# Kernel tuning notes

Hardware: AMD Instinct MI355X
Metric: run time of the kernel (lower is better)

Reference implementation:

```python
import jax, jax.numpy as jnp
import numpy as np

LN_EPS = 1e-5
N_FREQ = 10
D_TIME = 64
FIELD_DIMS = [(63, 128), (128, 128), (128, 3)]  # (d_in, d_out) per generated layer


def gelu(x):
    return jax.nn.gelu(x, approximate=False)  # torch default exact GELU


def ln(x, g, b):
    m = x.mean(-1, keepdims=True)
    v = ((x - m) ** 2).mean(-1, keepdims=True)
    return (x - m) / jnp.sqrt(v + LN_EPS) * g + b


def lin(x, w, b):
    return x @ w.T + b


def setup_inputs():
    key = jax.random.key(0)
    it = iter(jax.random.split(key, 64))

    def W(o, i, s=0.02):
        return jax.random.normal(next(it), (o, i), dtype=jnp.float32) * s

    inp = {}
    inp["points"] = jax.random.normal(next(it), (32, 16384, 3), dtype=jnp.float32)
    inp["t"] = jax.random.uniform(next(it), (32,), dtype=jnp.float32)
    # PointNet encoder: mlp1 = Lin(3,128)+LN+GELU+Lin(128,128)+LN+GELU
    inp["pn_w1"], inp["pn_b1"] = W(128, 3), jnp.zeros(128)
    inp["pn_g1"], inp["pn_be1"] = jnp.ones(128), jnp.zeros(128)
    inp["pn_w2"], inp["pn_b2"] = W(128, 128), jnp.zeros(128)
    inp["pn_g2"], inp["pn_be2"] = jnp.ones(128), jnp.zeros(128)
    # mlp2 = Lin(128,256)+LN+GELU+Lin(256,256)+LN
    inp["pn_w3"], inp["pn_b3"] = W(256, 128), jnp.zeros(256)
    inp["pn_g3"], inp["pn_be3"] = jnp.ones(256), jnp.zeros(256)
    inp["pn_w4"], inp["pn_b4"] = W(256, 256), jnp.zeros(256)
    inp["pn_g4"], inp["pn_be4"] = jnp.ones(256), jnp.zeros(256)
    # HyperNetwork context_proj: Lin(256+64,256)+LN+GELU+Lin(256,256)+LN+GELU
    inp["hp_w1"], inp["hp_b1"] = W(256, 320), jnp.zeros(256)
    inp["hp_g1"], inp["hp_be1"] = jnp.ones(256), jnp.zeros(256)
    inp["hp_w2"], inp["hp_b2"] = W(256, 256), jnp.zeros(256)
    inp["hp_g2"], inp["hp_be2"] = jnp.ones(256), jnp.zeros(256)
    # weight/bias generators for field dims [63,128,128,3]
    for i, (din, dout) in enumerate(FIELD_DIMS):
        inp[f"wg{i}_w"] = W(din * dout, 256)
        inp[f"wg{i}_b"] = jnp.zeros(din * dout)
        inp[f"bg{i}_w"] = W(dout, 256)
        inp[f"bg{i}_b"] = jnp.zeros(dout)
    return inp


def reference(points, t,
              pn_w1, pn_b1, pn_g1, pn_be1, pn_w2, pn_b2, pn_g2, pn_be2,
              pn_w3, pn_b3, pn_g3, pn_be3, pn_w4, pn_b4, pn_g4, pn_be4,
              hp_w1, hp_b1, hp_g1, hp_be1, hp_w2, hp_b2, hp_g2, hp_be2,
              wg0_w, wg0_b, bg0_w, bg0_b,
              wg1_w, wg1_b, bg1_w, bg1_b,
              wg2_w, wg2_b, bg2_w, bg2_b):
    B = points.shape[0]
    # ---- PointNet encoder -> global context [B, 256]
    h = gelu(ln(lin(points, pn_w1, pn_b1), pn_g1, pn_be1))
    h = gelu(ln(lin(h, pn_w2, pn_b2), pn_g2, pn_be2))
    h = gelu(ln(lin(h, pn_w3, pn_b3), pn_g3, pn_be3))
    h = ln(lin(h, pn_w4, pn_b4), pn_g4, pn_be4)
    ctx = h.max(axis=1)
    # ---- sinusoidal time embedding [B, 64]
    half = D_TIME // 2
    emb = jnp.exp(jnp.arange(half, dtype=jnp.float32) * (-np.log(10000.0) / (half - 1)))
    te = t[:, None] * emb
    te = jnp.concatenate([jnp.sin(te), jnp.cos(te)], axis=-1)
    # ---- hypernetwork context projection [B, 256]
    c = jnp.concatenate([ctx, te], axis=-1)
    c = gelu(ln(lin(c, hp_w1, hp_b1), hp_g1, hp_be1))
    c = gelu(ln(lin(c, hp_w2, hp_b2), hp_g2, hp_be2))
    # ---- Fourier position encoding [B, N, 63]
    freqs = (2.0 ** jnp.arange(N_FREQ, dtype=jnp.float32)) * jnp.pi
    xf = (points[..., None] * freqs).reshape(points.shape[0], points.shape[1], -1)
    pe = jnp.concatenate([points, jnp.sin(xf), jnp.cos(xf)], axis=-1)
    # ---- generate per-sample weights, apply field MLP
    gens = [(wg0_w, wg0_b, bg0_w, bg0_b), (wg1_w, wg1_b, bg1_w, bg1_b), (wg2_w, wg2_b, bg2_w, bg2_b)]
    x = pe
    n_layers = len(FIELD_DIMS)
    for i, ((din, dout), (wgw, wgb, bgw, bgb)) in enumerate(zip(FIELD_DIMS, gens)):
        w = lin(c, wgw, wgb).reshape(B, dout, din)
        w = w / jnp.maximum(jnp.linalg.norm(w, axis=-1, keepdims=True), 1e-12)  # F.normalize
        b = lin(c, bgw, bgb)
        x = jnp.einsum('bnd,bod->bno', x, w) + b[:, None, :]
        if i < n_layers - 1:
            x = gelu(x)
    return x  # [B, N, 3] velocities
```

## Files before the change

### kernel.cpp

```cpp
#include <hip/hip_runtime.h>

typedef _Float16 f16;
typedef f16 f16x8 __attribute__((ext_vector_type(8)));
typedef f16 f16x4 __attribute__((ext_vector_type(4)));
typedef float f32x4 __attribute__((ext_vector_type(4)));

#define N_PTS 16384
#define NBATCH 32
#define PTILE 64
#define PN_BLOCKS (N_PTS / PTILE)

__device__ __forceinline__ float gelu_exact(float x) {
    return 0.5f * x * (1.0f + erff(x * 0.70710678118654752440f));
}
__device__ __forceinline__ float gelu_fast(float x) {
    float u = x * x;
    float t = x * fmaf(u, 0.07135481627f, 1.5957691216f);
    float e = __expf(-t);
    return __fdividef(x, 1.f + e);
}
__device__ __forceinline__ unsigned fkey(float x) {
    unsigned u = __float_as_uint(x);
    return (u & 0x80000000u) ? ~u : (u | 0x80000000u);
}
__device__ __forceinline__ float funkey(unsigned k) {
    return (k & 0x80000000u) ? __uint_as_float(k ^ 0x80000000u) : __uint_as_float(~k);
}

template<int ACOLS, int DIN, int DOUT, int MODE>
__device__ __forceinline__ void mfma_layerT(
    f16 (*A)[ACOLS],
    const f16* __restrict__ Wg, const float* __restrict__ Bias,
    const float* __restrict__ Gam, const float* __restrict__ Bet,
    float2 (*Pp)[4], unsigned* __restrict__ mk)
{
    constexpr int KS = DIN / 32, TN = DOUT / 64;
    const int tid = threadIdx.x;
    const int w = tid >> 6, lane = tid & 63;
    const int i15 = lane & 15, g = lane >> 4;

    f32x4 d[4][TN];
#pragma unroll
    for (int nt = 0; nt < 4; ++nt)
#pragma unroll
        for (int mt = 0; mt < TN; ++mt) d[nt][mt] = (f32x4){0.f, 0.f, 0.f, 0.f};

#pragma unroll 2
    for (int ks = 0; ks < KS; ++ks) {
        f16x8 wf[TN];
#pragma unroll
        for (int mt = 0; mt < TN; ++mt)
            wf[mt] = *(const f16x8*)&Wg[(size_t)((w * TN + mt) * 16 + i15) * DIN + ks * 32 + g * 8];
#pragma unroll
        for (int nt = 0; nt < 4; ++nt) {
            f16x8 af = *(const f16x8*)&A[nt * 16 + i15][ks * 32 + g * 8];
#pragma unroll
            for (int mt = 0; mt < TN; ++mt)
                d[nt][mt] = __builtin_amdgcn_mfma_f32_16x16x32_f16(wf[mt], af, d[nt][mt], 0, 0, 0);
        }
    }

    float bi[TN][4], ga[TN][4], be[TN][4];
#pragma unroll
    for (int mt = 0; mt < TN; ++mt) {
        int cb = (w * TN + mt) * 16 + g * 4;
        *(float4*)bi[mt] = *(const float4*)&Bias[cb];
        if constexpr (MODE <= 1) {
            *(float4*)ga[mt] = *(const float4*)&Gam[cb];
            *(float4*)be[mt] = *(const float4*)&Bet[cb];
        }
    }
#pragma unroll
    for (int nt = 0; nt < 4; ++nt)
#pragma unroll
        for (int mt = 0; mt < TN; ++mt)
#pragma unroll
            for (int r = 0; r < 4; ++r) d[nt][mt][r] += bi[mt][r];

    if constexpr (MODE <= 1) {
#pragma unroll
        for (int nt = 0; nt < 4; ++nt) {
            float ss = 0.f, qq = 0.f;
#pragma unroll
            for (int mt = 0; mt < TN; ++mt)
#pragma unroll
                for (int r = 0; r < 4; ++r) {
                    float v = d[nt][mt][r];
                    ss += v; qq += v * v;
                }
            ss += __shfl_xor(ss, 16); qq += __shfl_xor(qq, 16);
            ss += __shfl_xor(ss, 32); qq += __shfl_xor(qq, 32);
            if (g == 0) Pp[nt * 16 + i15][w] = make_float2(ss, qq);
        }
        __syncthreads();
        float mx[TN][4];
        if constexpr (MODE == 1) {
#pragma unroll
            for (int mt = 0; mt < TN; ++mt)
#pragma unroll
                for (int r = 0; r < 4; ++r) mx[mt][r] = -1e30f;
        }
#pragma unroll
        for (int nt = 0; nt < 4; ++nt) {
            int pt = nt * 16 + i15;
            float4 pa = *(const float4*)&Pp[pt][0];
            float4 pb = *(const float4*)&Pp[pt][2];
            float S = pa.x + pa.z + pb.x + pb.z;
            float Q = pa.y + pa.w + pb.y + pb.w;
            float mean = S * (1.f / DOUT);
            float var = Q * (1.f / DOUT) - mean * mean;
            float rstd = rsqrtf(var + 1e-5f);
#pragma unroll
            for (int mt = 0; mt < TN; ++mt) {
                if constexpr (MODE == 0) {
                    f16x4 pk;
#pragma unroll
                    for (int r = 0; r < 4; ++r) {
                        float y = (d[nt][mt][r] - mean) * rstd * ga[mt][r] + be[mt][r];
                        pk[r] = (f16)gelu_fast(y);
                    }
                    *(f16x4*)&A[pt][(w * TN + mt) * 16 + g * 4] = pk;
                } else {
#pragma unroll
                    for (int r = 0; r < 4; ++r) {
                        float y = (d[nt][mt][r] - mean) * rstd * ga[mt][r] + be[mt][r];
                        mx[mt][r] = fmaxf(mx[mt][r], y);
                    }
                }
            }
        }
        if constexpr (MODE == 0) {
            __syncthreads();
        } else {
#pragma unroll
            for (int mt = 0; mt < TN; ++mt)
#pragma unroll
                for (int r = 0; r < 4; ++r) {
                    float m = mx[mt][r];
                    m = fmaxf(m, __shfl_xor(m, 1));
                    m = fmaxf(m, __shfl_xor(m, 2));
                    m = fmaxf(m, __shfl_xor(m, 4));
                    m = fmaxf(m, __shfl_xor(m, 8));
                    mx[mt][r] = m;
                }
            if (i15 == 0) {
#pragma unroll
                for (int mt = 0; mt < TN; ++mt)
#pragma unroll
                    for (int r = 0; r < 4; ++r)
                        atomicMax(&mk[(w * TN + mt) * 16 + g * 4 + r], fkey(mx[mt][r]));
            }
        }
    } else {
        __syncthreads();
#pragma unroll
        for (int nt = 0; nt < 4; ++nt) {
            int pt = nt * 16 + i15;
#pragma unroll
            for (int mt = 0; mt < TN; ++mt) {
                f16x4 pk;
#pragma unroll
                for (int r = 0; r < 4; ++r)
                    pk[r] = (f16)gelu_fast(d[nt][mt][r]);
                *(f16x4*)&A[pt][(w * TN + mt) * 16 + g * 4] = pk;
            }
        }
        __syncthreads();
    }
}

__global__ void init_kernel(unsigned* __restrict__ maxkey) {
    maxkey[blockIdx.x * 256 + threadIdx.x] = 0u;
}

__global__ void prep_kernel(const float* __restrict__ W1, const float* __restrict__ W2,
                            const float* __restrict__ W3, const float* __restrict__ W4,
                            f16* __restrict__ W1f, f16* __restrict__ W2f,
                            f16* __restrict__ W3f, f16* __restrict__ W4f) {
    int i = blockIdx.x * 256 + threadIdx.x;
    if (i < 128 * 32) {
        int r = i >> 5, c = i & 31;
        W1f[i] = (f16)(c < 3 ? W1[r * 3 + c] : 0.f);
    }
    int j = i - 128 * 32;
    if (j >= 0 && j < 128 * 128) W2f[j] = (f16)W2[j];
    int k = i - (128 * 32 + 128 * 128);
    if (k >= 0 && k < 256 * 128) W3f[k] = (f16)W3[k];
    int l = i - (128 * 32 + 128 * 128 + 256 * 128);
    if (l >= 0 && l < 256 * 256) W4f[l] = (f16)W4[l];
}

__global__ __launch_bounds__(256, 3)
void pointnet_kernel(const float* __restrict__ points,
                     const f16* __restrict__ W1f, const float* __restrict__ B1,
                     const float* __restrict__ G1, const float* __restrict__ E1,
                     const f16* __restrict__ W2f, const float* __restrict__ B2,
                     const float* __restrict__ G2, const float* __restrict__ E2,
                     const f16* __restrict__ W3f, const float* __restrict__ B3,
                     const float* __restrict__ G3, const float* __restrict__ E3,
                     const f16* __restrict__ W4f, const float* __restrict__ B4,
                     const float* __restrict__ G4, const float* __restrict__ E4,
                     unsigned* __restrict__ maxkey) {
    __shared__ __attribute__((aligned(16))) f16 A[PTILE][264];
    __shared__ float2 Pp[PTILE][4];
    const int b = blockIdx.x / PN_BLOCKS;
    const int n0 = (blockIdx.x % PN_BLOCKS) * PTILE;
    const int tid = threadIdx.x;
    for (int i = tid; i < PTILE * 32; i += 256) {
        int p = i >> 5, c = i & 31;
        A[p][c] = (f16)(c < 3 ? points[((size_t)b * N_PTS + n0 + p) * 3 + c] : 0.f);
    }
    __syncthreads();
    mfma_layerT<264, 32, 128, 0>(A, W1f, B1, G1, E1, Pp, nullptr);
    mfma_layerT<264, 128, 128, 0>(A, W2f, B2, G2, E2, Pp, nullptr);
    mfma_layerT<264, 128, 256, 0>(A, W3f, B3, G3, E3, Pp, nullptr);
    mfma_layerT<264, 256, 256, 1>(A, W4f, B4, G4, E4, Pp, maxkey + b * 256);
}

__global__ __launch_bounds__(256)
void hyper_kernel(const unsigned* __restrict__ maxkey, const float* __restrict__ tt,
                  const float* __restrict__ HW1, const float* __restrict__ HB1,
                  const float* __restrict__ HG1, const float* __restrict__ HE1,
                  const float* __restrict__ HW2, const float* __restrict__ HB2,
                  const float* __restrict__ HG2, const float* __restrict__ HE2,
                  float* __restrict__ c_out) {
    __shared__ float xc[320];
    __shared__ float buf[256];
    __shared__ float rs[4], rq[4];
    const int b = blockIdx.x, tid = threadIdx.x;
    xc[tid] = funkey(maxkey[b * 256 + tid]);
    if (tid < 32) {
        float emb = expf((float)tid * (-logf(10000.f) / 31.f));
        float arg = tt[b] * emb;
        xc[256 + tid] = sinf(arg);
        xc[288 + tid] = cosf(arg);
    }
    __syncthreads();
    float acc = HB1[tid];
    for (int i = 0; i < 320; i += 4) {
        float4 w = *(const float4*)&HW1[(size_t)tid * 320 + i];
        acc += xc[i] * w.x + xc[i + 1] * w.y + xc[i + 2] * w.z + xc[i + 3] * w.w;
    }
    float s = acc, q = acc * acc;
#pragma unroll
    for (int off = 32; off; off >>= 1) { s += __shfl_xor(s, off); q += __shfl_xor(q, off); }
    if ((tid & 63) == 0) { rs[tid >> 6] = s; rq[tid >> 6] = q; }
    __syncthreads();
    s = rs[0] + rs[1] + rs[2] + rs[3];
    q = rq[0] + rq[1] + rq[2] + rq[3];
    float mean = s * (1.f / 256), var = q * (1.f / 256) - mean * mean;
    float rstd = rsqrtf(var + 1e-5f);
    float h = gelu_exact((acc - mean) * rstd * HG1[tid] + HE1[tid]);
    __syncthreads();
    buf[tid] = h;
    __syncthreads();
    acc = HB2[tid];
    for (int i = 0; i < 256; i += 4) {
        float4 w = *(const float4*)&HW2[(size_t)tid * 256 + i];
        acc += buf[i] * w.x + buf[i + 1] * w.y + buf[i + 2] * w.z + buf[i + 3] * w.w;
    }
    s = acc; q = acc * acc;
#pragma unroll
    for (int off = 32; off; off >>= 1) { s += __shfl_xor(s, off); q += __shfl_xor(q, off); }
    if ((tid & 63) == 0) { rs[tid >> 6] = s; rq[tid >> 6] = q; }
    __syncthreads();
    s = rs[0] + rs[1] + rs[2] + rs[3];
    q = rq[0] + rq[1] + rq[2] + rq[3];
    mean = s * (1.f / 256); var = q * (1.f / 256) - mean * mean;
    rstd = rsqrtf(var + 1e-5f);
    c_out[b * 256 + tid] = gelu_exact((acc - mean) * rstd * HG2[tid] + HE2[tid]);
}

__device__ __forceinline__ void gen_row(float acc[32], const float (*cs)[256],
                                        const float* __restrict__ Wg,
                                        const float* __restrict__ Wgb, int f, bool valid) {
#pragma unroll
    for (int b = 0; b < 32; ++b) acc[b] = 0.f;
    if (!valid) return;
    for (int i = 0; i < 256; i += 4) {
        float4 w = *(const float4*)&Wg[(size_t)f * 256 + i];
#pragma unroll
        for (int b = 0; b < 32; ++b) {
            float4 cv = *(const float4*)&cs[b][i];
            acc[b] += cv.x * w.x + cv.y * w.y + cv.z * w.z + cv.w * w.w;
        }
    }
    float bias = Wgb[f];
#pragma unroll
    for (int b = 0; b < 32; ++b) acc[b] += bias;
}

__global__ __launch_bounds__(256)
void wgen_kernel(const float* __restrict__ c,
                 const float* __restrict__ WG0, const float* __restrict__ WGB0,
                 const float* __restrict__ BG0, const float* __restrict__ BGB0,
                 const float* __restrict__ WG1, const float* __restrict__ WGB1,
                 const float* __restrict__ BG1, const float* __restrict__ BGB1,
                 const float* __restrict__ WG2, const float* __restrict__ WGB2,
                 const float* __restrict__ BG2, const float* __restrict__ BGB2,
                 f16* __restrict__ w0f, f16* __restrict__ w1f, f16* __restrict__ w2f,
                 float* __restrict__ bb0, float* __restrict__ bb1, float* __restrict__ bb2) {
    __shared__ float cs[32][256];
    const int tid = threadIdx.x;
    for (int i = tid; i < 32 * 256; i += 256) cs[i >> 8][i & 255] = c[i];
    __syncthreads();
    const int wave = tid >> 6, lane = tid & 63;
    const int task = blockIdx.x * 4 + wave;
    if (task >= 262) return;

    float accA[32], accB[32];
    if (task < 259) {
        int layer, o;
        if (task < 128) { layer = 0; o = task; }
        else if (task < 256) { layer = 1; o = task - 128; }
        else { layer = 2; o = task - 256; }
        const int din = (layer == 0) ? 63 : 128;
        const float* Wg = (layer == 0) ? WG0 : (layer == 1) ? WG1 : WG2;
        const float* Wgb = (layer == 0) ? WGB0 : (layer == 1) ? WGB1 : WGB2;
        const int eA = lane, eB = lane + 64;
        const bool vA = eA < din, vB = eB < din;
        gen_row(accA, cs, Wg, Wgb, o * din + eA, vA);
        gen_row(accB, cs, Wg, Wgb, o * din + eB, vB);
#pragma unroll
        for (int b = 0; b < 32; ++b) {
            float xa = vA ? accA[b] : 0.f, xb = vB ? accB[b] : 0.f;
            float sq = xa * xa + xb * xb;
#pragma unroll
            for (int off = 32; off; off >>= 1) sq += __shfl_xor(sq, off);
            float rn = 1.f / fmaxf(sqrtf(sq), 1e-12f);
            if (layer == 0) {
                w0f[((size_t)b * 128 + o) * 64 + eA] = (f16)(vA ? accA[b] * rn : 0.f);
            } else if (layer == 1) {
                w1f[((size_t)b * 128 + o) * 128 + eA] = (f16)(accA[b] * rn);
                w1f[((size_t)b * 128 + o) * 128 + eB] = (f16)(accB[b] * rn);
            } else {
                w2f[((size_t)b * 3 + o) * 128 + eA] = (f16)(accA[b] * rn);
                w2f[((size_t)b * 3 + o) * 128 + eB] = (f16)(accB[b] * rn);
            }
        }
    } else {
        const int layer = task - 259;
        const int dout = (layer == 2) ? 3 : 128;
        const float* Bg = (layer == 0) ? BG0 : (layer == 1) ? BG1 : BG2;
        const float* Bgb = (layer == 0) ? BGB0 : (layer == 1) ? BGB1 : BGB2;
        const int eA = lane, eB = lane + 64;
        gen_row(accA, cs, Bg, Bgb, eA, eA < dout);
        gen_row(accB, cs, Bg, Bgb, eB, eB < dout);
        float* dst = (layer == 0) ? bb0 : (layer == 1) ? bb1 : bb2;
#pragma unroll
        for (int b = 0; b < 32; ++b) {
            if (eA < dout) dst[b * dout + eA] = accA[b];
            if (eB < dout) dst[b * dout + eB] = accB[b];
        }
    }
}

__global__ __launch_bounds__(256, 4)
void field_kernel(const float* __restrict__ points,
                  const f16* __restrict__ w0f, const float* __restrict__ bb0,
                  const f16* __restrict__ w1f, const float* __restrict__ bb1,
                  const f16* __restrict__ w2f, const float* __restrict__ bb2,
                  float* __restrict__ out) {
    __shared__ __attribute__((aligned(16))) f16 A[PTILE][136];
    const int b = blockIdx.x / PN_BLOCKS;
    const int n0 = (blockIdx.x % PN_BLOCKS) * PTILE;
    const int tid = threadIdx.x;
    {
        const int p = tid >> 2, q = tid & 3;
        float xyz[3];
#pragma unroll
        for (int dd = 0; dd < 3; ++dd)
            xyz[dd] = points[((size_t)b * N_PTS + n0 + p) * 3 + dd];
#pragma unroll
        for (int j = 0; j < 16; ++j) {
            int c = q * 16 + j;
            float val;
            if (c < 3) val = xyz[c];
            else if (c < 33) {
                int k = c - 3, dd = k / 10, f = k % 10;
                val = __sinf(xyz[dd] * ((float)(1 << f) * 3.14159265358979f));
            } else if (c < 63) {
                int k = c - 33, dd = k / 10, f = k % 10;
                val = __cosf(xyz[dd] * ((float)(1 << f) * 3.14159265358979f));
            } else val = 0.f;
            A[p][c] = (f16)val;
        }
    }
    __syncthreads();
    mfma_layerT<136, 64, 128, 2>(A, w0f + (size_t)b * 128 * 64, bb0 + b * 128,
                                 nullptr, nullptr, nullptr, nullptr);
    mfma_layerT<136, 128, 128, 2>(A, w1f + (size_t)b * 128 * 128, bb1 + b * 128,
                                  nullptr, nullptr, nullptr, nullptr);
    if (tid < PTILE * 3) {
        int p = tid / 3, ch = tid % 3;
        const f16* wr = w2f + ((size_t)b * 3 + ch) * 128;
        float acc = 0.f;
        for (int k = 0; k < 128; k += 8) {
            f16x8 av = *(const f16x8*)&A[p][k];
            f16x8 wv = *(const f16x8*)&wr[k];
#pragma unroll
            for (int j = 0; j < 8; ++j) acc += (float)av[j] * (float)wv[j];
        }
        out[((size_t)b * N_PTS + n0 + p) * 3 + ch] = acc + bb2[b * 3 + ch];
    }
}

extern "C" void kernel_launch(void* const* d_in, const int* in_sizes, int n_in,
                              void* d_out, int out_size, void* d_ws, size_t ws_size,
                              hipStream_t stream) {
    const float* points = (const float*)d_in[0];
    const float* tt = (const float*)d_in[1];
    const float* pw1 = (const float*)d_in[2],  *pb1 = (const float*)d_in[3];
    const float* pg1 = (const float*)d_in[4],  *pe1 = (const float*)d_in[5];
    const float* pw2 = (const float*)d_in[6],  *pb2 = (const float*)d_in[7];
    const float* pg2 = (const float*)d_in[8],  *pe2 = (const float*)d_in[9];
    const float* pw3 = (const float*)d_in[10], *pb3 = (const float*)d_in[11];
    const float* pg3 = (const float*)d_in[12], *pe3 = (const float*)d_in[13];
    const float* pw4 = (const float*)d_in[14], *pb4 = (const float*)d_in[15];
    const float* pg4 = (const float*)d_in[16], *pe4 = (const float*)d_in[17];
    const float* hw1 = (const float*)d_in[18], *hb1 = (const float*)d_in[19];
    const float* hg1 = (const float*)d_in[20], *he1 = (const float*)d_in[21];
    const float* hw2 = (const float*)d_in[22], *hb2 = (const float*)d_in[23];
    const float* hg2 = (const float*)d_in[24], *he2 = (const float*)d_in[25];
    const float* wg0w = (const float*)d_in[26], *wg0b = (const float*)d_in[27];
    const float* bg0w = (const float*)d_in[28], *bg0b = (const float*)d_in[29];
    const float* wg1w = (const float*)d_in[30], *wg1b = (const float*)d_in[31];
    const float* bg1w = (const float*)d_in[32], *bg1b = (const float*)d_in[33];
    const float* wg2w = (const float*)d_in[34], *wg2b = (const float*)d_in[35];
    const float* bg2w = (const float*)d_in[36], *bg2b = (const float*)d_in[37];

    char* p = (char*)d_ws;
    unsigned* maxkey = (unsigned*)p;           p += 8192 * 4;
    float* c_buf = (float*)p;                  p += 8192 * 4;
    float* bb0 = (float*)p;                    p += 4096 * 4;
    float* bb1 = (float*)p;                    p += 4096 * 4;
    float* bb2 = (float*)p;                    p += 96 * 4 + 64;
    f16* W1f = (f16*)p;                        p += 128 * 32 * 2;
    f16* W2f = (f16*)p;                        p += 128 * 128 * 2;
    f16* W3f = (f16*)p;                        p += 256 * 128 * 2;
    f16* W4f = (f16*)p;                        p += 256 * 256 * 2;
    f16* w0f = (f16*)p;                        p += (size_t)32 * 128 * 64 * 2;
    f16* w1f = (f16*)p;                        p += (size_t)32 * 128 * 128 * 2;
    f16* w2f = (f16*)p;                        p += (size_t)32 * 3 * 128 * 2;

    init_kernel<<<32, 256, 0, stream>>>(maxkey);
    prep_kernel<<<464, 256, 0, stream>>>(pw1, pw2, pw3, pw4, W1f, W2f, W3f, W4f);
    pointnet_kernel<<<NBATCH * PN_BLOCKS, 256, 0, stream>>>(
        points, W1f, pb1, pg1, pe1, W2f, pb2, pg2, pe2,
        W3f, pb3, pg3, pe3, W4f, pb4, pg4, pe4, maxkey);
    hyper_kernel<<<NBATCH, 256, 0, stream>>>(
        maxkey, tt, hw1, hb1, hg1, he1, hw2, hb2, hg2, he2, c_buf);
    wgen_kernel<<<66, 256, 0, stream>>>(
        c_buf, wg0w, wg0b, bg0w, bg0b, wg1w, wg1b, bg1w, bg1b,
        wg2w, wg2b, bg2w, bg2b, w0f, w1f, w2f, bb0, bb1, bb2);
    field_kernel<<<NBATCH * PN_BLOCKS, 256, 0, stream>>>(
        points, w0f, bb0, w1f, bb1, w2f, bb2, (float*)d_out);
}
```

Measured before the change: 831.7 us.

## Compute LayerNorm affine and GELU in packed half2 arithmetic, raise occupancy bounds

Replaces the fp32 sigmoid-based GELU with a packed __half2 version using exp2 and rcp, and performs the LayerNorm scale/shift in half2 for the non-max layers. It also loads gamma/beta only where needed to cut register pressure, raises launch_bounds occupancy for the pointnet and field kernels, and vectorizes the initial points tile load. The goal is to halve elementwise ALU cost in the epilogues and fit more waves per CU. The cost is lower precision in the normalization and activation, plus possible spills under the tighter register limits.

```diff
diff --git a/kernel.cpp b/kernel.cpp
--- a/kernel.cpp
+++ b/kernel.cpp
@@ -1,4 +1,5 @@
 #include <hip/hip_runtime.h>
+#include <hip/hip_fp16.h>
 
 typedef _Float16 f16;
 typedef f16 f16x8 __attribute__((ext_vector_type(8)));
@@ -13,11 +14,14 @@
 __device__ __forceinline__ float gelu_exact(float x) {
     return 0.5f * x * (1.0f + erff(x * 0.70710678118654752440f));
 }
-__device__ __forceinline__ float gelu_fast(float x) {
-    float u = x * x;
-    float t = x * fmaf(u, 0.07135481627f, 1.5957691216f);
-    float e = __expf(-t);
-    return __fdividef(x, 1.f + e);
+__device__ __forceinline__ __half2 gelu_pk(__half2 x) {
+    const __half2 c1 = __float2half2_rn(-0.10293984f);
+    const __half2 c2 = __float2half2_rn(-2.30220830f);
+    const __half2 one = __float2half2_rn(1.0f);
+    __half2 u = __hmul2(x, x);
+    __half2 t = __hmul2(x, __hfma2(u, c1, c2));
+    __half2 e = h2exp2(t);
+    return __hmul2(x, h2rcp(__hadd2(e, one)));
 }
 __device__ __forceinline__ unsigned fkey(float x) {
     unsigned u = __float_as_uint(x);
@@ -60,22 +64,18 @@
         }
     }
 
-    float bi[TN][4], ga[TN][4], be[TN][4];
-#pragma unroll
-    for (int mt = 0; mt < TN; ++mt) {
-        int cb = (w * TN + mt) * 16 + g * 4;
-        *(float4*)bi[mt] = *(const float4*)&Bias[cb];
-        if constexpr (MODE <= 1) {
-            *(float4*)ga[mt] = *(const float4*)&Gam[cb];
-            *(float4*)be[mt] = *(const float4*)&Bet[cb];
-        }
-    }
-#pragma unroll
-    for (int nt = 0; nt < 4; ++nt)
+    {
+        float bi[TN][4];
 #pragma unroll
         for (int mt = 0; mt < TN; ++mt)
-#pragma unroll
-            for (int r = 0; r < 4; ++r) d[nt][mt][r] += bi[mt][r];
+            *(float4*)bi[mt] = *(const float4*)&Bias[(w * TN + mt) * 16 + g * 4];
+#pragma unroll
+        for (int nt = 0; nt < 4; ++nt)
+#pragma unroll
+            for (int mt = 0; mt < TN; ++mt)
+#pragma unroll
+                for (int r = 0; r < 4; ++r) d[nt][mt][r] += bi[mt][r];
+    }
 
     if constexpr (MODE <= 1) {
 #pragma unroll
@@ -93,45 +93,76 @@
             if (g == 0) Pp[nt * 16 + i15][w] = make_float2(ss, qq);
         }
         __syncthreads();
-        float mx[TN][4];
-        if constexpr (MODE == 1) {
+
+        if constexpr (MODE == 0) {
+            __half2 gh[TN][2], beh[TN][2];
+#pragma unroll
+            for (int mt = 0; mt < TN; ++mt) {
+                int cb = (w * TN + mt) * 16 + g * 4;
+                float4 gv = *(const float4*)&Gam[cb];
+                float4 bv = *(const float4*)&Bet[cb];
+                gh[mt][0] = __floats2half2_rn(gv.x, gv.y);
+                gh[mt][1] = __floats2half2_rn(gv.z, gv.w);
+                beh[mt][0] = __floats2half2_rn(bv.x, bv.y);
+                beh[mt][1] = __floats2half2_rn(bv.z, bv.w);
+            }
+#pragma unroll
+            for (int nt = 0; nt < 4; ++nt) {
+                int pt = nt * 16 + i15;
+                float4 pa = *(const float4*)&Pp[pt][0];
+                float4 pb = *(const float4*)&Pp[pt][2];
+                float S = pa.x + pa.z + pb.x + pb.z;
+                float Q = pa.y + pa.w + pb.y + pb.w;
+                float mean = S * (1.f / DOUT);
+                float var = Q * (1.f / DOUT) - mean * mean;
+                float rstd = rsqrtf(var + 1e-5f);
+                __half2 r2 = __float2half2_rn(rstd);
+                __half2 nm2 = __float2half2_rn(-mean);
+#pragma unroll
+                for (int mt = 0; mt < TN; ++mt) {
+                    union { f16x4 v; __half2 h[2]; } u;
+#pragma unroll
+                    for (int j = 0; j < 2; ++j) {
+                        __half2 xb = __floats2half2_rn(d[nt][mt][2 * j], d[nt][mt][2 * j + 1]);
+                        __half2 k1 = __hmul2(r2, gh[mt][j]);
+                        __half2 k2 = __hfma2(nm2, k1, beh[mt][j]);
+                        u.h[j] = gelu_pk(__hfma2(xb, k1, k2));
+                    }
+                    *(f16x4*)&A[pt][(w * TN + mt) * 16 + g * 4] = u.v;
+                }
+            }
+            __syncthreads();
+        } else {
+            float ga[TN][4], be[TN][4];
+#pragma unroll
+            for (int mt = 0; mt < TN; ++mt) {
+                int cb = (w * TN + mt) * 16 + g * 4;
+                *(float4*)ga[mt] = *(const float4*)&Gam[cb];
+                *(float4*)be[mt] = *(const float4*)&Bet[cb];
+            }
+            float mx[TN][4];
 #pragma unroll
             for (int mt = 0; mt < TN; ++mt)
 #pragma unroll
                 for (int r = 0; r < 4; ++r) mx[mt][r] = -1e30f;
-        }
-#pragma unroll
-        for (int nt = 0; nt < 4; ++nt) {
-            int pt = nt * 16 + i15;
-            float4 pa = *(const float4*)&Pp[pt][0];
-            float4 pb = *(const float4*)&Pp[pt][2];
-            float S = pa.x + pa.z + pb.x + pb.z;
-            float Q = pa.y + pa.w + pb.y + pb.w;
-            float mean = S * (1.f / DOUT);
-            float var = Q * (1.f / DOUT) - mean * mean;
-            float rstd = rsqrtf(var + 1e-5f);
-#pragma unroll
-            for (int mt = 0; mt < TN; ++mt) {
-                if constexpr (MODE == 0) {
-                    f16x4 pk;
-#pragma unroll
-                    for (int r = 0; r < 4; ++r) {
-                        float y = (d[nt][mt][r] - mean) * rstd * ga[mt][r] + be[mt][r];
-                        pk[r] = (f16)gelu_fast(y);
-                    }
-                    *(f16x4*)&A[pt][(w * TN + mt) * 16 + g * 4] = pk;
-                } else {
+#pragma unroll
+            for (int nt = 0; nt < 4; ++nt) {
+                int pt = nt * 16 + i15;
+                float4 pa = *(const float4*)&Pp[pt][0];
+                float4 pb = *(const float4*)&Pp[pt][2];
+                float S = pa.x + pa.z + pb.x + pb.z;
+                float Q = pa.y + pa.w + pb.y + pb.w;
+                float mean = S * (1.f / DOUT);
+                float var = Q * (1.f / DOUT) - mean * mean;
+                float rstd = rsqrtf(var + 1e-5f);
+#pragma unroll
+                for (int mt = 0; mt < TN; ++mt)
 #pragma unroll
                     for (int r = 0; r < 4; ++r) {
                         float y = (d[nt][mt][r] - mean) * rstd * ga[mt][r] + be[mt][r];
                         mx[mt][r] = fmaxf(mx[mt][r], y);
                     }
-                }
-            }
-        }
-        if constexpr (MODE == 0) {
-            __syncthreads();
-        } else {
+            }
 #pragma unroll
             for (int mt = 0; mt < TN; ++mt)
 #pragma unroll
@@ -158,11 +189,10 @@
             int pt = nt * 16 + i15;
 #pragma unroll
             for (int mt = 0; mt < TN; ++mt) {
-                f16x4 pk;
-#pragma unroll
-                for (int r = 0; r < 4; ++r)
-                    pk[r] = (f16)gelu_fast(d[nt][mt][r]);
-                *(f16x4*)&A[pt][(w * TN + mt) * 16 + g * 4] = pk;
+                union { f16x4 v; __half2 h[2]; } u;
+                u.h[0] = gelu_pk(__floats2half2_rn(d[nt][mt][0], d[nt][mt][1]));
+                u.h[1] = gelu_pk(__floats2half2_rn(d[nt][mt][2], d[nt][mt][3]));
+                *(f16x4*)&A[pt][(w * TN + mt) * 16 + g * 4] = u.v;
             }
         }
         __syncthreads();
@@ -190,7 +220,7 @@
     if (l >= 0 && l < 256 * 256) W4f[l] = (f16)W4[l];
 }
 
-__global__ __launch_bounds__(256, 3)
+__global__ __launch_bounds__(256, 4)
 void pointnet_kernel(const float* __restrict__ points,
                      const f16* __restrict__ W1f, const float* __restrict__ B1,
                      const float* __restrict__ G1, const float* __restrict__ E1,
@@ -206,9 +236,15 @@
     const int b = blockIdx.x / PN_BLOCKS;
     const int n0 = (blockIdx.x % PN_BLOCKS) * PTILE;
     const int tid = threadIdx.x;
-    for (int i = tid; i < PTILE * 32; i += 256) {
-        int p = i >> 5, c = i & 31;
-        A[p][c] = (f16)(c < 3 ? points[((size_t)b * N_PTS + n0 + p) * 3 + c] : 0.f);
+    if (tid < PTILE) {
+        const float* ps = &points[((size_t)b * N_PTS + n0 + tid) * 3];
+        f16x8 v = {};
+        v[0] = (f16)ps[0]; v[1] = (f16)ps[1]; v[2] = (f16)ps[2];
+        *(f16x8*)&A[tid][0] = v;
+    } else {
+        int idx = tid - PTILE, r = idx / 3, sg = idx % 3 + 1;
+        f16x8 z = {};
+        *(f16x8*)&A[r][sg * 8] = z;
     }
     __syncthreads();
     mfma_layerT<264, 32, 128, 0>(A, W1f, B1, G1, E1, Pp, nullptr);
@@ -355,7 +391,7 @@
     }
 }
 
-__global__ __launch_bounds__(256, 4)
+__global__ __launch_bounds__(256, 5)
 void field_kernel(const float* __restrict__ points,
                   const f16* __restrict__ w0f, const float* __restrict__ bb0,
                   const f16* __restrict__ w1f, const float* __restrict__ bb1,
```

Result: faster. 775.3 us (-6.8%).
